# Kernel optimization log

Measured on AMD Instinct MI355X. Metric: run time of the kernel, lower is better.

The kernel has to match this reference:

```python
import jax, jax.numpy as jnp
import numpy as np

B, N = 16, 300000          # batch, total anchors per image (all FPN levels concatenated)
PRE, POST = 2000, 1000     # num_pre_nms, num_post_nms
NMS_THR = 0.7
MIN_SIZE = 1e-3            # proposal_min_size
IMG_H, IMG_W = 800.0, 1333.0


def setup_inputs() -> dict:
    key = jax.random.key(0)
    k1, k2, k3, k4, k5, k6 = jax.random.split(key, 6)
    cls = jax.random.normal(k1, (B, N), dtype=jnp.float32)
    reg = jax.random.normal(k2, (B, N, 4), dtype=jnp.float32) * 0.1
    # anchors as valid (cx,cy,w,h)->(x1,y1,x2,y2) boxes inside the image
    cx = jax.random.uniform(k3, (B, N), dtype=jnp.float32, minval=0.0, maxval=IMG_W)
    cy = jax.random.uniform(k4, (B, N), dtype=jnp.float32, minval=0.0, maxval=IMG_H)
    w = jax.random.uniform(k5, (B, N), dtype=jnp.float32, minval=16.0, maxval=256.0)
    h = jax.random.uniform(k6, (B, N), dtype=jnp.float32, minval=16.0, maxval=256.0)
    anchors = jnp.stack([cx - 0.5 * w, cy - 0.5 * h, cx + 0.5 * w, cy + 0.5 * h], axis=-1)
    return {"cls": cls, "reg": reg, "anchors": anchors}


def _decode(anchor, reg):
    aw = anchor[:, 2] - anchor[:, 0]
    ah = anchor[:, 3] - anchor[:, 1]
    acx = anchor[:, 0] + 0.5 * aw
    acy = anchor[:, 1] + 0.5 * ah
    dx, dy, dw, dh = reg[:, 0], reg[:, 1], reg[:, 2], reg[:, 3]
    pcx = dx * aw + acx
    pcy = dy * ah + acy
    pw = jnp.exp(dw) * aw
    ph = jnp.exp(dh) * ah
    return jnp.stack([pcx - 0.5 * pw, pcy - 0.5 * ph, pcx + 0.5 * pw, pcy + 0.5 * ph], axis=-1)


def _iou_matrix(boxes):
    # boxes: [K,4] -> pairwise IoU [K,K]
    area = (boxes[:, 2] - boxes[:, 0]) * (boxes[:, 3] - boxes[:, 1])
    lt = jnp.maximum(boxes[:, None, :2], boxes[None, :, :2])
    rb = jnp.minimum(boxes[:, None, 2:], boxes[None, :, 2:])
    wh = jnp.clip(rb - lt, 0.0)
    inter = wh[..., 0] * wh[..., 1]
    union = area[:, None] + area[None, :] - inter
    return inter / jnp.maximum(union, 1e-8)


def _per_image(score, reg, anchor):
    # topk pre-NMS selection (lax.top_k returns score-descending order)
    top_s, idx = jax.lax.top_k(score, PRE)
    boxes = _decode(anchor[idx], reg[idx].reshape(-1, 4))
    # clip to image bounds
    bounds = jnp.array([IMG_W, IMG_H, IMG_W, IMG_H], dtype=boxes.dtype)
    boxes = jnp.clip(boxes, 0.0, bounds)
    # remove small boxes (mask instead of dynamic removal)
    w = boxes[:, 2] - boxes[:, 0]
    h = boxes[:, 3] - boxes[:, 1]
    valid = (w >= MIN_SIZE) & (h >= MIN_SIZE)
    s = jnp.where(valid, top_s, -jnp.inf)
    order = jnp.argsort(-s)  # score-descending, invalid last
    boxes = boxes[order]
    valid = valid[order]
    # greedy NMS: iterate highest-score-first, suppress later boxes with IoU > thr
    iou = _iou_matrix(boxes)
    rng = jnp.arange(PRE)
    def body(i, keep):
        sup = (iou[i] > NMS_THR) & keep[i]
        return keep & jnp.logical_not(sup & (rng > i))
    keep = jax.lax.fori_loop(0, PRE, body, valid)
    # gather kept boxes (score order preserved), pad with zeros past count
    sel = jnp.argsort(jnp.logical_not(keep), stable=True)[:POST]
    return boxes[sel] * keep[sel][:, None].astype(boxes.dtype)


def reference(cls, reg, anchors):
    # [B, POST, 4] proposals per image (zero-padded where fewer than POST kept)
    return jax.vmap(_per_image)(cls, reg, anchors)
```

## Files before the change

### kernel.cpp

```cpp
#include <hip/hip_runtime.h>

#define NB 16
#define NN 300000
#define PRE 2000
#define POST 1000

typedef unsigned long long ull;

static const size_t OFF_HIST1   = 0;
static const size_t OFF_HIST2   = 65536;
static const size_t OFF_HIST3   = 196608;
static const size_t OFF_CANDCNT = 327680;
static const size_t OFF_EQCNT   = 327936;
static const size_t OFF_BITMAP  = 328192;
static const size_t OFF_B1      = 332288;
static const size_t OFF_NEED1   = 332544;
static const size_t OFF_B2      = 332800;
static const size_t OFF_NEED2   = 333056;
static const size_t OFF_B3      = 333312;
static const size_t OFF_NEED3   = 333568;
static const size_t OFF_NVALID  = 333824;
static const size_t ZERO_BYTES  = 334080;
static const size_t OFF_CAND    = 334080;
static const size_t OFF_EQBUF   = 465152;
static const size_t OFF_KEYS    = 989440;
static const size_t OFF_BOXTMP  = 1251584;
static const size_t OFF_SORTED  = 1775872;
static const size_t OFF_MASK    = 2287872;

__device__ __forceinline__ unsigned f2u(float f){
  unsigned b = __float_as_uint(f);
  return (b & 0x80000000u) ? ~b : (b | 0x80000000u);
}

#define H1REP 8
#define H1STRIDE 1025
__global__ void k_hist1(const float* __restrict__ cls, unsigned* __restrict__ hist){
  __shared__ unsigned h[H1REP * H1STRIDE];
  int img = blockIdx.y;
  for (int i = threadIdx.x; i < H1REP * H1STRIDE; i += blockDim.x) h[i] = 0;
  __syncthreads();
  const float* p = cls + (size_t)img * NN;
  int stride = gridDim.x * blockDim.x;
  unsigned rep = (threadIdx.x & (H1REP - 1)) * H1STRIDE;
  for (int i = blockIdx.x * blockDim.x + threadIdx.x; i < NN; i += stride)
    atomicAdd(&h[rep + (f2u(p[i]) >> 22)], 1u);
  __syncthreads();
  unsigned* g = hist + img * 1024;
  for (int i = threadIdx.x; i < 1024; i += blockDim.x){
    unsigned v = 0;
    for (int r = 0; r < H1REP; r++) v += h[r * H1STRIDE + i];
    if (v) atomicAdd(&g[i], v);
  }
}

__global__ void k_scan(const unsigned* __restrict__ hist, int bins,
                       const unsigned* __restrict__ tgt, unsigned K0,
                       unsigned* __restrict__ outBin, unsigned* __restrict__ outNeed){
  int img = blockIdx.x;
  int t = threadIdx.x;
  const unsigned* hh = hist + img * bins;
  unsigned K = tgt ? tgt[img] : K0;
  int per = bins >> 8;
  unsigned s = 0;
  for (int q = 0; q < per; q++) s += hh[bins - 1 - (t * per + q)];
  __shared__ unsigned arr[256];
  arr[t] = s;
  __syncthreads();
  for (int off = 1; off < 256; off <<= 1){
    unsigned v = (t >= off) ? arr[t - off] : 0u;
    __syncthreads();
    arr[t] += v;
    __syncthreads();
  }
  unsigned incl = arr[t], excl = incl - s;
  if (excl < K && K <= incl){
    unsigned c = excl;
    for (int q = 0; q < per; q++){
      int b = bins - 1 - (t * per + q);
      unsigned cnt = hh[b];
      if (c + cnt >= K){ outBin[img] = (unsigned)b; outNeed[img] = K - c; break; }
      c += cnt;
    }
  }
}

__global__ void k_hist2(const float* __restrict__ cls, const unsigned* __restrict__ b1,
                        unsigned* __restrict__ hist){
  int img = blockIdx.y;
  unsigned bb1 = b1[img];
  const float* p = cls + (size_t)img * NN;
  unsigned* g = hist + img * 2048;
  int stride = gridDim.x * blockDim.x;
  for (int i = blockIdx.x * blockDim.x + threadIdx.x; i < NN; i += stride){
    unsigned u = f2u(p[i]);
    if ((u >> 22) == bb1) atomicAdd(&g[(u >> 11) & 0x7FFu], 1u);
  }
}

__global__ void k_hist3(const float* __restrict__ cls, const unsigned* __restrict__ b1,
                        const unsigned* __restrict__ b2, unsigned* __restrict__ hist){
  int img = blockIdx.y;
  unsigned pref = (b1[img] << 11) | b2[img];
  const float* p = cls + (size_t)img * NN;
  unsigned* g = hist + img * 2048;
  int stride = gridDim.x * blockDim.x;
  for (int i = blockIdx.x * blockDim.x + threadIdx.x; i < NN; i += stride){
    unsigned u = f2u(p[i]);
    if ((u >> 11) == pref) atomicAdd(&g[u & 0x7FFu], 1u);
  }
}

__global__ void k_compact(const float* __restrict__ cls, const unsigned* __restrict__ b1,
                          const unsigned* __restrict__ b2, const unsigned* __restrict__ b3,
                          unsigned* __restrict__ cand, unsigned* __restrict__ candCnt,
                          unsigned* __restrict__ eqbuf, unsigned* __restrict__ eqCnt){
  __shared__ unsigned lc[1024];
  __shared__ unsigned le[256];
  __shared__ unsigned lcn, len_, baseC, baseE;
  int img = blockIdx.y;
  if (threadIdx.x == 0){ lcn = 0; len_ = 0; }
  __syncthreads();
  unsigned T = (b1[img] << 22) | (b2[img] << 11) | b3[img];
  const float* p = cls + (size_t)img * NN;
  int stride = gridDim.x * blockDim.x;
  for (int i = blockIdx.x * blockDim.x + threadIdx.x; i < NN; i += stride){
    unsigned u = f2u(p[i]);
    if (u > T){
      unsigned pos = atomicAdd(&lcn, 1u);
      if (pos < 1024u) lc[pos] = (unsigned)i;
      else { unsigned g = atomicAdd(&candCnt[img], 1u); if (g < 2048u) cand[img * 2048 + g] = (unsigned)i; }
    } else if (u == T){
      unsigned pos = atomicAdd(&len_, 1u);
      if (pos < 256u) le[pos] = (unsigned)i;
      else { unsigned g = atomicAdd(&eqCnt[img], 1u); if (g < 8192u) eqbuf[img * 8192 + g] = (unsigned)i; }
    }
  }
  __syncthreads();
  unsigned nc = lcn < 1024u ? lcn : 1024u;
  unsigned ne = len_ < 256u ? len_ : 256u;
  if (threadIdx.x == 0){
    if (nc) baseC = atomicAdd(&candCnt[img], nc);
    if (ne) baseE = atomicAdd(&eqCnt[img], ne);
  }
  __syncthreads();
  for (unsigned t = threadIdx.x; t < nc; t += blockDim.x){
    unsigned g = baseC + t;
    if (g < 2048u) cand[img * 2048 + g] = lc[t];
  }
  for (unsigned t = threadIdx.x; t < ne; t += blockDim.x){
    unsigned g = baseE + t;
    if (g < 8192u) eqbuf[img * 8192 + g] = le[t];
  }
}

__global__ void k_finalize(unsigned* __restrict__ cand, const unsigned* __restrict__ candCnt,
                           const unsigned* __restrict__ eqbuf, const unsigned* __restrict__ eqCnt,
                           const unsigned* __restrict__ need3){
  int img = blockIdx.x, tid = threadIdx.x;
  unsigned need = need3[img];
  unsigned ec = eqCnt[img]; if (ec > 8192u) ec = 8192u;
  unsigned base = candCnt[img];
  const unsigned* eq = eqbuf + img * 8192;
  unsigned* c = cand + img * 2048;
  if (need >= ec){
    for (unsigned t = tid; t < ec; t += 256) if (base + t < 2048u) c[base + t] = eq[t];
    return;
  }
  for (unsigned t = tid; t < ec; t += 256){
    unsigned v = eq[t], r = 0;
    for (unsigned s = 0; s < ec; s++) r += (eq[s] < v) ? 1u : 0u;
    if (r < need && base + r < 2048u) c[base + r] = v;
  }
}

__global__ void k_decode(const float* __restrict__ cls, const float* __restrict__ reg,
                         const float* __restrict__ anch, const unsigned* __restrict__ cand,
                         float* __restrict__ boxTmp, ull* __restrict__ keys,
                         unsigned* __restrict__ nvalid){
  int s = blockIdx.x * blockDim.x + threadIdx.x;
  if (s >= NB * 2048) return;
  int img = s >> 11, slot = s & 2047;
  ull key = 0ull;
  float4 box = make_float4(0.f, 0.f, 0.f, 0.f);
  bool counted = false;
  if (slot < PRE){
    unsigned i = cand[img * 2048 + slot];
    if (i < NN){
      size_t gi = (size_t)img * NN + i;
      float4 a = ((const float4*)anch)[gi];
      float4 r = ((const float4*)reg)[gi];
      float sc = cls[gi];
      float aw = a.z - a.x, ah = a.w - a.y;
      float acx = a.x + 0.5f * aw, acy = a.y + 0.5f * ah;
      float pcx = r.x * aw + acx, pcy = r.y * ah + acy;
      float pw = expf(r.z) * aw, ph = expf(r.w) * ah;
      float x1 = pcx - 0.5f * pw, y1 = pcy - 0.5f * ph;
      float x2 = pcx + 0.5f * pw, y2 = pcy + 0.5f * ph;
      x1 = fminf(fmaxf(x1, 0.f), 1333.f); x2 = fminf(fmaxf(x2, 0.f), 1333.f);
      y1 = fminf(fmaxf(y1, 0.f), 800.f);  y2 = fminf(fmaxf(y2, 0.f), 800.f);
      bool valid = ((x2 - x1) >= 0.001f) && ((y2 - y1) >= 0.001f);
      unsigned up = valid ? f2u(sc) : 0u;
      key = ((ull)up << 32) | (ull)(0xFFFFFFFFu - i);
      box = make_float4(x1, y1, x2, y2);
      counted = valid;
    }
  }
  keys[img * 2048 + slot] = key;
  ((float4*)boxTmp)[img * 2048 + slot] = box;
  ull bal = __ballot(counted);
  if ((threadIdx.x & 63) == 0 && bal)
    atomicAdd(&nvalid[img], (unsigned)__popcll(bal));
}

__global__ __launch_bounds__(256) void k_rank(const ull* __restrict__ keys,
                                              const float* __restrict__ boxTmp,
                                              float* __restrict__ sorted){
  __shared__ ull lk[2048];
  int img = blockIdx.y;
  int e = blockIdx.x * 256 + threadIdx.x;
  for (int t = threadIdx.x; t < 2048; t += 256) lk[t] = keys[img * 2048 + t];
  __syncthreads();
  ull me = lk[e];
  unsigned rank = 0;
  #pragma unroll 8
  for (int j = 0; j < 2048; j++) rank += (lk[j] > me) ? 1u : 0u;
  if (rank < PRE)
    ((float4*)sorted)[img * PRE + rank] = ((const float4*)boxTmp)[img * 2048 + e];
}

__global__ __launch_bounds__(512) void k_mask(const float* __restrict__ sorted,
                                              const unsigned* __restrict__ nvalid,
                                              ull* __restrict__ mask, ull* __restrict__ bitmap){
  __shared__ float4 bx[PRE];
  __shared__ float  ar[PRE];
  __shared__ unsigned rowflag[16];
  int img = blockIdx.y, tid = threadIdx.x;
  if (tid < 16) rowflag[tid] = 0;
  for (int i = tid; i < PRE; i += 512){
    float4 b = ((const float4*)sorted)[img * PRE + i];
    bx[i] = b;
    ar[i] = (b.z - b.x) * (b.w - b.y);
  }
  __syncthreads();
  int row = blockIdx.x * 16 + (tid >> 5);
  int w = tid & 31;
  float4 bi = bx[row];
  float ai = ar[row];
  int qlo = (row >= w) ? (((row - w) >> 5) + 1) : 0;
  int qhi = ((PRE - 1 - w) >> 5) + 1;
  ull m = 0;
  for (int q = qlo; q < qhi; q++){
    int j = (q << 5) + w;
    float4 bj = bx[j];
    float xx1 = fmaxf(bi.x, bj.x), yy1 = fmaxf(bi.y, bj.y);
    float xx2 = fminf(bi.z, bj.z), yy2 = fminf(bi.w, bj.w);
    float ww = fmaxf(xx2 - xx1, 0.f), hh = fmaxf(yy2 - yy1, 0.f);
    float inter = ww * hh;
    float uni = ai + ar[j] - inter;
    if (inter / fmaxf(uni, 1e-8f) > 0.7f) m |= (1ull << q);
  }
  mask[((size_t)(img * PRE + row)) * 32 + w] = m;
  if (m) atomicOr(&rowflag[tid >> 5], 1u);
  __syncthreads();
  if (tid < 16){
    int r = blockIdx.x * 16 + tid;
    if (rowflag[tid] && r < (int)nvalid[img])
      atomicOr(&bitmap[img * 32 + (r >> 6)], 1ull << (r & 63));
  }
}

#define CHR 48
__global__ __launch_bounds__(256) void k_nms(const ull* __restrict__ mask,
                                             const ull* __restrict__ bitmap,
                                             const unsigned* __restrict__ nvalid,
                                             const float* __restrict__ sorted,
                                             float* __restrict__ out){
  __shared__ unsigned rowsLds[2048];
  __shared__ unsigned cntw[32];
  __shared__ unsigned wbaseS[32];
  __shared__ int mcountS, mpS;
  __shared__ ull cacheD[2][CHR * 32];
  __shared__ ull keepP[32];
  __shared__ ull keepLin[32];
  __shared__ unsigned cntArr[32], preArr[32];
  int img = blockIdx.x, tid = threadIdx.x;
  int lane = tid & 63, wave = tid >> 6;

  if (tid < 32) cntw[tid] = (unsigned)__popcll(bitmap[img * 32 + tid]);
  __syncthreads();
  if (tid == 0){
    unsigned s = 0;
    for (int w0 = 0; w0 < 32; w0++){ wbaseS[w0] = s; s += cntw[w0]; }
    mcountS = (int)s;
    mpS = ((int)s + CHR - 1) / CHR * CHR;
  }
  __syncthreads();
  int m = mcountS, mp = mpS;
  if (tid < 32){
    ull bits = bitmap[img * 32 + tid];
    unsigned pos = wbaseS[tid];
    int base_i = tid * 64;
    while (bits){
      int b = __ffsll((long long)bits) - 1;
      rowsLds[pos++] = (unsigned)(base_i + b);
      bits &= bits - 1;
    }
  }
  for (int t = m + tid; t < mp; t += 256) rowsLds[t] = PRE - 1;
  __syncthreads();

  int nch = mp / CHR;
  ull remv = 0;
  const ull* mg = mask + (size_t)img * PRE * 32;

  if (nch > 0 && tid >= 64){
    int s = tid - 64;
    ull v[8];
    #pragma unroll
    for (int k = 0; k < 8; k++){
      int t = k * 192 + s;
      unsigned rr = rowsLds[t >> 5];
      v[k] = mg[(size_t)rr * 32 + (t & 31)];
    }
    #pragma unroll
    for (int k = 0; k < 8; k++) cacheD[0][k * 192 + s] = v[k];
  }
  __syncthreads();

  for (int c = 0; c < nch; c++){
    int cb = c & 1;
    if (tid >= 64){
      if (c + 1 < nch){
        int q0n = (c + 1) * CHR;
        int s = tid - 64;
        ull v[8];
        #pragma unroll
        for (int k = 0; k < 8; k++){
          int t = k * 192 + s;
          unsigned rr = rowsLds[q0n + (t >> 5)];
          v[k] = mg[(size_t)rr * 32 + (t & 31)];
        }
        #pragma unroll
        for (int k = 0; k < 8; k++) cacheD[cb ^ 1][k * 192 + s] = v[k];
      }
    } else {
      const ull* cbuf = cacheD[cb];
      const int q0 = c * CHR;
      ull cur[8]; unsigned ci[8];
      #pragma unroll
      for (int k = 0; k < 8; k++){
        ci[k] = rowsLds[q0 + k];
        cur[k] = cbuf[(k << 5) | (lane & 31)];
      }
      #pragma unroll
      for (int g = 0; g < 6; g++){
        ull nxt[8]; unsigned ni[8];
        if (g < 5){
          #pragma unroll
          for (int k = 0; k < 8; k++){
            int lq = (g + 1) * 8 + k;
            ni[k] = rowsLds[q0 + lq];
            nxt[k] = cbuf[(lq << 5) | (lane & 31)];
          }
        }
        #pragma unroll
        for (int k = 0; k < 8; k++){
          unsigned i = ci[k];
          unsigned bit = ((unsigned)(remv >> (i >> 5))) & 1u;
          int sup = (lane == (int)(i & 31)) && bit;
          if (!__any(sup)) remv |= cur[k];
        }
        if (g < 5){
          #pragma unroll
          for (int k = 0; k < 8; k++){ cur[k] = nxt[k]; ci[k] = ni[k]; }
        }
      }
    }
    __syncthreads();
  }

  int nv = (int)nvalid[img];
  if (wave == 0 && lane < 32){
    int cnt2 = (nv > lane) ? (((nv - 1 - lane) >> 5) + 1) : 0;
    ull vm = (cnt2 >= 64) ? ~0ull : ((1ull << cnt2) - 1ull);
    keepP[lane] = (~remv) & vm;
  }
  __syncthreads();
  if (tid < 32){
    ull lin = 0;
    for (int kk = 0; kk < 64; kk++)
      lin |= ((keepP[kk & 31] >> (2 * tid + (kk >> 5))) & 1ull) << kk;
    keepLin[tid] = lin;
    cntArr[tid] = (unsigned)__popcll(lin);
  }
  __syncthreads();
  if (tid < 32){
    unsigned pre = 0;
    for (int w0 = 0; w0 < tid; w0++) pre += cntArr[w0];
    preArr[tid] = pre;
  }
  __syncthreads();
  for (int i = tid; i < PRE; i += 256){
    int w0 = i >> 6, b = i & 63;
    ull kw = keepLin[w0];
    if ((kw >> b) & 1ull){
      unsigned rank = preArr[w0] + (unsigned)__popcll(kw & ((1ull << b) - 1ull));
      if (rank < POST)
        ((float4*)out)[img * POST + rank] = ((const float4*)sorted)[img * PRE + i];
    }
  }
}

extern "C" void kernel_launch(void* const* d_in, const int* in_sizes, int n_in,
                              void* d_out, int out_size, void* d_ws, size_t ws_size,
                              hipStream_t stream){
  const float* cls  = (const float*)d_in[0];
  const float* reg  = (const float*)d_in[1];
  const float* anch = (const float*)d_in[2];
  float* out = (float*)d_out;
  char* ws = (char*)d_ws;

  unsigned* hist1   = (unsigned*)(ws + OFF_HIST1);
  unsigned* hist2   = (unsigned*)(ws + OFF_HIST2);
  unsigned* hist3   = (unsigned*)(ws + OFF_HIST3);
  unsigned* candCnt = (unsigned*)(ws + OFF_CANDCNT);
  unsigned* eqCnt   = (unsigned*)(ws + OFF_EQCNT);
  ull*      bitmap  = (ull*)     (ws + OFF_BITMAP);
  unsigned* b1      = (unsigned*)(ws + OFF_B1);
  unsigned* need1   = (unsigned*)(ws + OFF_NEED1);
  unsigned* b2      = (unsigned*)(ws + OFF_B2);
  unsigned* need2   = (unsigned*)(ws + OFF_NEED2);
  unsigned* b3      = (unsigned*)(ws + OFF_B3);
  unsigned* need3   = (unsigned*)(ws + OFF_NEED3);
  unsigned* nvalid  = (unsigned*)(ws + OFF_NVALID);
  unsigned* cand    = (unsigned*)(ws + OFF_CAND);
  unsigned* eqbuf   = (unsigned*)(ws + OFF_EQBUF);
  ull*      keys    = (ull*)     (ws + OFF_KEYS);
  float*    boxTmp  = (float*)   (ws + OFF_BOXTMP);
  float*    sorted  = (float*)   (ws + OFF_SORTED);
  ull*      mask    = (ull*)     (ws + OFF_MASK);

  hipMemsetAsync(ws, 0, ZERO_BYTES, stream);
  hipMemsetAsync(d_out, 0, (size_t)out_size * sizeof(float), stream);

  k_hist1<<<dim3(64, NB), 256, 0, stream>>>(cls, hist1);
  k_scan <<<NB, 256, 0, stream>>>(hist1, 1024, (const unsigned*)nullptr, 2000u, b1, need1);
  k_hist2<<<dim3(64, NB), 256, 0, stream>>>(cls, b1, hist2);
  k_scan <<<NB, 256, 0, stream>>>(hist2, 2048, need1, 0u, b2, need2);
  k_hist3<<<dim3(64, NB), 256, 0, stream>>>(cls, b1, b2, hist3);
  k_scan <<<NB, 256, 0, stream>>>(hist3, 2048, need2, 0u, b3, need3);
  k_compact<<<dim3(64, NB), 256, 0, stream>>>(cls, b1, b2, b3, cand, candCnt, eqbuf, eqCnt);
  k_finalize<<<NB, 256, 0, stream>>>(cand, candCnt, eqbuf, eqCnt, need3);
  k_decode<<<(NB * 2048) / 256, 256, 0, stream>>>(cls, reg, anch, cand, boxTmp, keys, nvalid);
  k_rank<<<dim3(8, NB), 256, 0, stream>>>(keys, boxTmp, sorted);
  k_mask<<<dim3(PRE / 16, NB), 512, 0, stream>>>(sorted, nvalid, mask, bitmap);
  k_nms<<<NB, 256, 0, stream>>>(mask, bitmap, nvalid, sorted, out);
}
```

Baseline: 305.3 us.

## Fuse all pipeline stages into one cooperative persistent kernel with grid syncs

Replaces the twelve separate launches and the memsets with a single cooperative kernel of 768 blocks. Stages are separated by grid-wide syncs, and each stage reuses one shared-memory buffer. The mask stage is spread over 48 blocks per image. The aim is to remove per-launch overhead and idle gaps between many small kernels, at the cost of grid-sync latency and fixed occupancy limits.

```diff
diff --git a/kernel.cpp b/kernel.cpp
--- a/kernel.cpp
+++ b/kernel.cpp
@@ -1,70 +1,69 @@
 #include <hip/hip_runtime.h>
+#include <hip/hip_cooperative_groups.h>
+
+namespace cg = cooperative_groups;
 
 #define NB 16
 #define NN 300000
 #define PRE 2000
 #define POST 1000
+#define GRID 768
+#define BLK 256
+#define BPI 48
+#define CHR 48
 
 typedef unsigned long long ull;
 
-static const size_t OFF_HIST1   = 0;
-static const size_t OFF_HIST2   = 65536;
-static const size_t OFF_HIST3   = 196608;
-static const size_t OFF_CANDCNT = 327680;
-static const size_t OFF_EQCNT   = 327936;
-static const size_t OFF_BITMAP  = 328192;
-static const size_t OFF_B1      = 332288;
-static const size_t OFF_NEED1   = 332544;
-static const size_t OFF_B2      = 332800;
-static const size_t OFF_NEED2   = 333056;
-static const size_t OFF_B3      = 333312;
-static const size_t OFF_NEED3   = 333568;
-static const size_t OFF_NVALID  = 333824;
-static const size_t ZERO_BYTES  = 334080;
-static const size_t OFF_CAND    = 334080;
-static const size_t OFF_EQBUF   = 465152;
-static const size_t OFF_KEYS    = 989440;
-static const size_t OFF_BOXTMP  = 1251584;
-static const size_t OFF_SORTED  = 1775872;
-static const size_t OFF_MASK    = 2287872;
+static constexpr size_t OFF_HIST1   = 0;
+static constexpr size_t OFF_HIST2   = 65536;
+static constexpr size_t OFF_HIST3   = 196608;
+static constexpr size_t OFF_CANDCNT = 327680;
+static constexpr size_t OFF_EQCNT   = 327936;
+static constexpr size_t OFF_BITMAP  = 328192;
+static constexpr size_t OFF_B1      = 332288;
+static constexpr size_t OFF_NEED1   = 332544;
+static constexpr size_t OFF_B2      = 332800;
+static constexpr size_t OFF_NEED2   = 333056;
+static constexpr size_t OFF_B3      = 333312;
+static constexpr size_t OFF_NEED3   = 333568;
+static constexpr size_t OFF_NVALID  = 333824;
+static constexpr size_t ZERO_BYTES  = 334080;
+static constexpr size_t OFF_CAND    = 334080;
+static constexpr size_t OFF_EQBUF   = 465152;
+static constexpr size_t OFF_KEYS    = 989440;
+static constexpr size_t OFF_BOXTMP  = 1251584;
+static constexpr size_t OFF_SORTED  = 1775872;
+static constexpr size_t OFF_MASK    = 2287872;
 
 __device__ __forceinline__ unsigned f2u(float f){
   unsigned b = __float_as_uint(f);
   return (b & 0x80000000u) ? ~b : (b | 0x80000000u);
 }
 
-#define H1REP 8
-#define H1STRIDE 1025
-__global__ void k_hist1(const float* __restrict__ cls, unsigned* __restrict__ hist){
-  __shared__ unsigned h[H1REP * H1STRIDE];
-  int img = blockIdx.y;
-  for (int i = threadIdx.x; i < H1REP * H1STRIDE; i += blockDim.x) h[i] = 0;
-  __syncthreads();
-  const float* p = cls + (size_t)img * NN;
-  int stride = gridDim.x * blockDim.x;
-  unsigned rep = (threadIdx.x & (H1REP - 1)) * H1STRIDE;
-  for (int i = blockIdx.x * blockDim.x + threadIdx.x; i < NN; i += stride)
-    atomicAdd(&h[rep + (f2u(p[i]) >> 22)], 1u);
-  __syncthreads();
-  unsigned* g = hist + img * 1024;
-  for (int i = threadIdx.x; i < 1024; i += blockDim.x){
-    unsigned v = 0;
-    for (int r = 0; r < H1REP; r++) v += h[r * H1STRIDE + i];
-    if (v) atomicAdd(&g[i], v);
-  }
-}
-
-__global__ void k_scan(const unsigned* __restrict__ hist, int bins,
-                       const unsigned* __restrict__ tgt, unsigned K0,
-                       unsigned* __restrict__ outBin, unsigned* __restrict__ outNeed){
-  int img = blockIdx.x;
-  int t = threadIdx.x;
+struct CompactS { unsigned lc[1024]; unsigned le[256]; unsigned lcn, len_, baseC, baseE; };
+struct NmsS {
+  unsigned rowsLds[2048];
+  unsigned cntw[32];
+  unsigned wbaseS[32];
+  int mcountS, mpS;
+  ull cacheD[2][CHR * 32];
+  ull keepP[32];
+  ull keepLin[32];
+  unsigned cntArr[32], preArr[32];
+};
+static_assert(sizeof(CompactS) <= 40448, "compact lds");
+static_assert(sizeof(NmsS)     <= 40448, "nms lds");
+
+__device__ void dev_scan(const unsigned* __restrict__ hist, int bins,
+                         const unsigned* __restrict__ tgt, unsigned K0,
+                         unsigned* __restrict__ outBin, unsigned* __restrict__ outNeed,
+                         char* sm, int img, int t){
+  unsigned* arr = (unsigned*)sm;
   const unsigned* hh = hist + img * bins;
   unsigned K = tgt ? tgt[img] : K0;
   int per = bins >> 8;
   unsigned s = 0;
   for (int q = 0; q < per; q++) s += hh[bins - 1 - (t * per + q)];
-  __shared__ unsigned arr[256];
   arr[t] = s;
   __syncthreads();
   for (int off = 1; off < 256; off <<= 1){
@@ -85,341 +84,16 @@
   }
 }
 
-__global__ void k_hist2(const float* __restrict__ cls, const unsigned* __restrict__ b1,
-                        unsigned* __restrict__ hist){
-  int img = blockIdx.y;
-  unsigned bb1 = b1[img];
-  const float* p = cls + (size_t)img * NN;
-  unsigned* g = hist + img * 2048;
-  int stride = gridDim.x * blockDim.x;
-  for (int i = blockIdx.x * blockDim.x + threadIdx.x; i < NN; i += stride){
-    unsigned u = f2u(p[i]);
-    if ((u >> 22) == bb1) atomicAdd(&g[(u >> 11) & 0x7FFu], 1u);
-  }
-}
-
-__global__ void k_hist3(const float* __restrict__ cls, const unsigned* __restrict__ b1,
-                        const unsigned* __restrict__ b2, unsigned* __restrict__ hist){
-  int img = blockIdx.y;
-  unsigned pref = (b1[img] << 11) | b2[img];
-  const float* p = cls + (size_t)img * NN;
-  unsigned* g = hist + img * 2048;
-  int stride = gridDim.x * blockDim.x;
-  for (int i = blockIdx.x * blockDim.x + threadIdx.x; i < NN; i += stride){
-    unsigned u = f2u(p[i]);
-    if ((u >> 11) == pref) atomicAdd(&g[u & 0x7FFu], 1u);
-  }
-}
-
-__global__ void k_compact(const float* __restrict__ cls, const unsigned* __restrict__ b1,
-                          const unsigned* __restrict__ b2, const unsigned* __restrict__ b3,
-                          unsigned* __restrict__ cand, unsigned* __restrict__ candCnt,
-                          unsigned* __restrict__ eqbuf, unsigned* __restrict__ eqCnt){
-  __shared__ unsigned lc[1024];
-  __shared__ unsigned le[256];
-  __shared__ unsigned lcn, len_, baseC, baseE;
-  int img = blockIdx.y;
-  if (threadIdx.x == 0){ lcn = 0; len_ = 0; }
-  __syncthreads();
-  unsigned T = (b1[img] << 22) | (b2[img] << 11) | b3[img];
-  const float* p = cls + (size_t)img * NN;
-  int stride = gridDim.x * blockDim.x;
-  for (int i = blockIdx.x * blockDim.x + threadIdx.x; i < NN; i += stride){
-    unsigned u = f2u(p[i]);
-    if (u > T){
-      unsigned pos = atomicAdd(&lcn, 1u);
-      if (pos < 1024u) lc[pos] = (unsigned)i;
-      else { unsigned g = atomicAdd(&candCnt[img], 1u); if (g < 2048u) cand[img * 2048 + g] = (unsigned)i; }
-    } else if (u == T){
-      unsigned pos = atomicAdd(&len_, 1u);
-      if (pos < 256u) le[pos] = (unsigned)i;
-      else { unsigned g = atomicAdd(&eqCnt[img], 1u); if (g < 8192u) eqbuf[img * 8192 + g] = (unsigned)i; }
-    }
-  }
-  __syncthreads();
-  unsigned nc = lcn < 1024u ? lcn : 1024u;
-  unsigned ne = len_ < 256u ? len_ : 256u;
-  if (threadIdx.x == 0){
-    if (nc) baseC = atomicAdd(&candCnt[img], nc);
-    if (ne) baseE = atomicAdd(&eqCnt[img], ne);
-  }
-  __syncthreads();
-  for (unsigned t = threadIdx.x; t < nc; t += blockDim.x){
-    unsigned g = baseC + t;
-    if (g < 2048u) cand[img * 2048 + g] = lc[t];
-  }
-  for (unsigned t = threadIdx.x; t < ne; t += blockDim.x){
-    unsigned g = baseE + t;
-    if (g < 8192u) eqbuf[img * 8192 + g] = le[t];
-  }
-}
-
-__global__ void k_finalize(unsigned* __restrict__ cand, const unsigned* __restrict__ candCnt,
-                           const unsigned* __restrict__ eqbuf, const unsigned* __restrict__ eqCnt,
-                           const unsigned* __restrict__ need3){
-  int img = blockIdx.x, tid = threadIdx.x;
-  unsigned need = need3[img];
-  unsigned ec = eqCnt[img]; if (ec > 8192u) ec = 8192u;
-  unsigned base = candCnt[img];
-  const unsigned* eq = eqbuf + img * 8192;
-  unsigned* c = cand + img * 2048;
-  if (need >= ec){
-    for (unsigned t = tid; t < ec; t += 256) if (base + t < 2048u) c[base + t] = eq[t];
-    return;
-  }
-  for (unsigned t = tid; t < ec; t += 256){
-    unsigned v = eq[t], r = 0;
-    for (unsigned s = 0; s < ec; s++) r += (eq[s] < v) ? 1u : 0u;
-    if (r < need && base + r < 2048u) c[base + r] = v;
-  }
-}
-
-__global__ void k_decode(const float* __restrict__ cls, const float* __restrict__ reg,
-                         const float* __restrict__ anch, const unsigned* __restrict__ cand,
-                         float* __restrict__ boxTmp, ull* __restrict__ keys,
-                         unsigned* __restrict__ nvalid){
-  int s = blockIdx.x * blockDim.x + threadIdx.x;
-  if (s >= NB * 2048) return;
-  int img = s >> 11, slot = s & 2047;
-  ull key = 0ull;
-  float4 box = make_float4(0.f, 0.f, 0.f, 0.f);
-  bool counted = false;
-  if (slot < PRE){
-    unsigned i = cand[img * 2048 + slot];
-    if (i < NN){
-      size_t gi = (size_t)img * NN + i;
-      float4 a = ((const float4*)anch)[gi];
-      float4 r = ((const float4*)reg)[gi];
-      float sc = cls[gi];
-      float aw = a.z - a.x, ah = a.w - a.y;
-      float acx = a.x + 0.5f * aw, acy = a.y + 0.5f * ah;
-      float pcx = r.x * aw + acx, pcy = r.y * ah + acy;
-      float pw = expf(r.z) * aw, ph = expf(r.w) * ah;
-      float x1 = pcx - 0.5f * pw, y1 = pcy - 0.5f * ph;
-      float x2 = pcx + 0.5f * pw, y2 = pcy + 0.5f * ph;
-      x1 = fminf(fmaxf(x1, 0.f), 1333.f); x2 = fminf(fmaxf(x2, 0.f), 1333.f);
-      y1 = fminf(fmaxf(y1, 0.f), 800.f);  y2 = fminf(fmaxf(y2, 0.f), 800.f);
-      bool valid = ((x2 - x1) >= 0.001f) && ((y2 - y1) >= 0.001f);
-      unsigned up = valid ? f2u(sc) : 0u;
-      key = ((ull)up << 32) | (ull)(0xFFFFFFFFu - i);
-      box = make_float4(x1, y1, x2, y2);
-      counted = valid;
-    }
-  }
-  keys[img * 2048 + slot] = key;
-  ((float4*)boxTmp)[img * 2048 + slot] = box;
-  ull bal = __ballot(counted);
-  if ((threadIdx.x & 63) == 0 && bal)
-    atomicAdd(&nvalid[img], (unsigned)__popcll(bal));
-}
-
-__global__ __launch_bounds__(256) void k_rank(const ull* __restrict__ keys,
-                                              const float* __restrict__ boxTmp,
-                                              float* __restrict__ sorted){
-  __shared__ ull lk[2048];
-  int img = blockIdx.y;
-  int e = blockIdx.x * 256 + threadIdx.x;
-  for (int t = threadIdx.x; t < 2048; t += 256) lk[t] = keys[img * 2048 + t];
-  __syncthreads();
-  ull me = lk[e];
-  unsigned rank = 0;
-  #pragma unroll 8
-  for (int j = 0; j < 2048; j++) rank += (lk[j] > me) ? 1u : 0u;
-  if (rank < PRE)
-    ((float4*)sorted)[img * PRE + rank] = ((const float4*)boxTmp)[img * 2048 + e];
-}
-
-__global__ __launch_bounds__(512) void k_mask(const float* __restrict__ sorted,
-                                              const unsigned* __restrict__ nvalid,
-                                              ull* __restrict__ mask, ull* __restrict__ bitmap){
-  __shared__ float4 bx[PRE];
-  __shared__ float  ar[PRE];
-  __shared__ unsigned rowflag[16];
-  int img = blockIdx.y, tid = threadIdx.x;
-  if (tid < 16) rowflag[tid] = 0;
-  for (int i = tid; i < PRE; i += 512){
-    float4 b = ((const float4*)sorted)[img * PRE + i];
-    bx[i] = b;
-    ar[i] = (b.z - b.x) * (b.w - b.y);
-  }
-  __syncthreads();
-  int row = blockIdx.x * 16 + (tid >> 5);
-  int w = tid & 31;
-  float4 bi = bx[row];
-  float ai = ar[row];
-  int qlo = (row >= w) ? (((row - w) >> 5) + 1) : 0;
-  int qhi = ((PRE - 1 - w) >> 5) + 1;
-  ull m = 0;
-  for (int q = qlo; q < qhi; q++){
-    int j = (q << 5) + w;
-    float4 bj = bx[j];
-    float xx1 = fmaxf(bi.x, bj.x), yy1 = fmaxf(bi.y, bj.y);
-    float xx2 = fminf(bi.z, bj.z), yy2 = fminf(bi.w, bj.w);
-    float ww = fmaxf(xx2 - xx1, 0.f), hh = fmaxf(yy2 - yy1, 0.f);
-    float inter = ww * hh;
-    float uni = ai + ar[j] - inter;
-    if (inter / fmaxf(uni, 1e-8f) > 0.7f) m |= (1ull << q);
-  }
-  mask[((size_t)(img * PRE + row)) * 32 + w] = m;
-  if (m) atomicOr(&rowflag[tid >> 5], 1u);
-  __syncthreads();
-  if (tid < 16){
-    int r = blockIdx.x * 16 + tid;
-    if (rowflag[tid] && r < (int)nvalid[img])
-      atomicOr(&bitmap[img * 32 + (r >> 6)], 1ull << (r & 63));
-  }
-}
-
-#define CHR 48
-__global__ __launch_bounds__(256) void k_nms(const ull* __restrict__ mask,
-                                             const ull* __restrict__ bitmap,
-                                             const unsigned* __restrict__ nvalid,
-                                             const float* __restrict__ sorted,
-                                             float* __restrict__ out){
-  __shared__ unsigned rowsLds[2048];
-  __shared__ unsigned cntw[32];
-  __shared__ unsigned wbaseS[32];
-  __shared__ int mcountS, mpS;
-  __shared__ ull cacheD[2][CHR * 32];
-  __shared__ ull keepP[32];
-  __shared__ ull keepLin[32];
-  __shared__ unsigned cntArr[32], preArr[32];
-  int img = blockIdx.x, tid = threadIdx.x;
-  int lane = tid & 63, wave = tid >> 6;
-
-  if (tid < 32) cntw[tid] = (unsigned)__popcll(bitmap[img * 32 + tid]);
-  __syncthreads();
-  if (tid == 0){
-    unsigned s = 0;
-    for (int w0 = 0; w0 < 32; w0++){ wbaseS[w0] = s; s += cntw[w0]; }
-    mcountS = (int)s;
-    mpS = ((int)s + CHR - 1) / CHR * CHR;
-  }
-  __syncthreads();
-  int m = mcountS, mp = mpS;
-  if (tid < 32){
-    ull bits = bitmap[img * 32 + tid];
-    unsigned pos = wbaseS[tid];
-    int base_i = tid * 64;
-    while (bits){
-      int b = __ffsll((long long)bits) - 1;
-      rowsLds[pos++] = (unsigned)(base_i + b);
-      bits &= bits - 1;
-    }
-  }
-  for (int t = m + tid; t < mp; t += 256) rowsLds[t] = PRE - 1;
-  __syncthreads();
-
-  int nch = mp / CHR;
-  ull remv = 0;
-  const ull* mg = mask + (size_t)img * PRE * 32;
-
-  if (nch > 0 && tid >= 64){
-    int s = tid - 64;
-    ull v[8];
-    #pragma unroll
-    for (int k = 0; k < 8; k++){
-      int t = k * 192 + s;
-      unsigned rr = rowsLds[t >> 5];
-      v[k] = mg[(size_t)rr * 32 + (t & 31)];
-    }
-    #pragma unroll
-    for (int k = 0; k < 8; k++) cacheD[0][k * 192 + s] = v[k];
-  }
-  __syncthreads();
-
-  for (int c = 0; c < nch; c++){
-    int cb = c & 1;
-    if (tid >= 64){
-      if (c + 1 < nch){
-        int q0n = (c + 1) * CHR;
-        int s = tid - 64;
-        ull v[8];
-        #pragma unroll
-        for (int k = 0; k < 8; k++){
-          int t = k * 192 + s;
-          unsigned rr = rowsLds[q0n + (t >> 5)];
-          v[k] = mg[(size_t)rr * 32 + (t & 31)];
-        }
-        #pragma unroll
-        for (int k = 0; k < 8; k++) cacheD[cb ^ 1][k * 192 + s] = v[k];
-      }
-    } else {
-      const ull* cbuf = cacheD[cb];
-      const int q0 = c * CHR;
-      ull cur[8]; unsigned ci[8];
-      #pragma unroll
-      for (int k = 0; k < 8; k++){
-        ci[k] = rowsLds[q0 + k];
-        cur[k] = cbuf[(k << 5) | (lane & 31)];
-      }
-      #pragma unroll
-      for (int g = 0; g < 6; g++){
-        ull nxt[8]; unsigned ni[8];
-        if (g < 5){
-          #pragma unroll
-          for (int k = 0; k < 8; k++){
-            int lq = (g + 1) * 8 + k;
-            ni[k] = rowsLds[q0 + lq];
-            nxt[k] = cbuf[(lq << 5) | (lane & 31)];
-          }
-        }
-        #pragma unroll
-        for (int k = 0; k < 8; k++){
-          unsigned i = ci[k];
-          unsigned bit = ((unsigned)(remv >> (i >> 5))) & 1u;
-          int sup = (lane == (int)(i & 31)) && bit;
-          if (!__any(sup)) remv |= cur[k];
-        }
-        if (g < 5){
-          #pragma unroll
-          for (int k = 0; k < 8; k++){ cur[k] = nxt[k]; ci[k] = ni[k]; }
-        }
-      }
-    }
-    __syncthreads();
-  }
-
-  int nv = (int)nvalid[img];
-  if (wave == 0 && lane < 32){
-    int cnt2 = (nv > lane) ? (((nv - 1 - lane) >> 5) + 1) : 0;
-    ull vm = (cnt2 >= 64) ? ~0ull : ((1ull << cnt2) - 1ull);
-    keepP[lane] = (~remv) & vm;
-  }
-  __syncthreads();
-  if (tid < 32){
-    ull lin = 0;
-    for (int kk = 0; kk < 64; kk++)
-      lin |= ((keepP[kk & 31] >> (2 * tid + (kk >> 5))) & 1ull) << kk;
-    keepLin[tid] = lin;
-    cntArr[tid] = (unsigned)__popcll(lin);
-  }
-  __syncthreads();
-  if (tid < 32){
-    unsigned pre = 0;
-    for (int w0 = 0; w0 < tid; w0++) pre += cntArr[w0];
-    preArr[tid] = pre;
-  }
-  __syncthreads();
-  for (int i = tid; i < PRE; i += 256){
-    int w0 = i >> 6, b = i & 63;
-    ull kw = keepLin[w0];
-    if ((kw >> b) & 1ull){
-      unsigned rank = preArr[w0] + (unsigned)__popcll(kw & ((1ull << b) - 1ull));
-      if (rank < POST)
-        ((float4*)out)[img * POST + rank] = ((const float4*)sorted)[img * PRE + i];
-    }
-  }
-}
-
-extern "C" void kernel_launch(void* const* d_in, const int* in_sizes, int n_in,
-                              void* d_out, int out_size, void* d_ws, size_t ws_size,
-                              hipStream_t stream){
-  const float* cls  = (const float*)d_in[0];
-  const float* reg  = (const float*)d_in[1];
-  const float* anch = (const float*)d_in[2];
-  float* out = (float*)d_out;
-  char* ws = (char*)d_ws;
+__global__ __launch_bounds__(BLK, 3) void mega(const float* __restrict__ cls,
+                                               const float* __restrict__ reg,
+                                               const float* __restrict__ anch,
+                                               float* __restrict__ out,
+                                               char* __restrict__ ws,
+                                               int outFloats){
+  __shared__ __align__(16) char sm[40448];
+  cg::grid_group gg = cg::this_grid();
+  const int bid = blockIdx.x, tid = threadIdx.x;
+  const int gtid = bid * BLK + tid;
 
   unsigned* hist1   = (unsigned*)(ws + OFF_HIST1);
   unsigned* hist2   = (unsigned*)(ws + OFF_HIST2);
@@ -439,21 +113,359 @@
   ull*      keys    = (ull*)     (ws + OFF_KEYS);
   float*    boxTmp  = (float*)   (ws + OFF_BOXTMP);
   float*    sorted  = (float*)   (ws + OFF_SORTED);
-  ull*      mask    = (ull*)     (ws + OFF_MASK);
-
-  hipMemsetAsync(ws, 0, ZERO_BYTES, stream);
-  hipMemsetAsync(d_out, 0, (size_t)out_size * sizeof(float), stream);
-
-  k_hist1<<<dim3(64, NB), 256, 0, stream>>>(cls, hist1);
-  k_scan <<<NB, 256, 0, stream>>>(hist1, 1024, (const unsigned*)nullptr, 2000u, b1, need1);
-  k_hist2<<<dim3(64, NB), 256, 0, stream>>>(cls, b1, hist2);
-  k_scan <<<NB, 256, 0, stream>>>(hist2, 2048, need1, 0u, b2, need2);
-  k_hist3<<<dim3(64, NB), 256, 0, stream>>>(cls, b1, b2, hist3);
-  k_scan <<<NB, 256, 0, stream>>>(hist3, 2048, need2, 0u, b3, need3);
-  k_compact<<<dim3(64, NB), 256, 0, stream>>>(cls, b1, b2, b3, cand, candCnt, eqbuf, eqCnt);
-  k_finalize<<<NB, 256, 0, stream>>>(cand, candCnt, eqbuf, eqCnt, need3);
-  k_decode<<<(NB * 2048) / 256, 256, 0, stream>>>(cls, reg, anch, cand, boxTmp, keys, nvalid);
-  k_rank<<<dim3(8, NB), 256, 0, stream>>>(keys, boxTmp, sorted);
-  k_mask<<<dim3(PRE / 16, NB), 512, 0, stream>>>(sorted, nvalid, mask, bitmap);
-  k_nms<<<NB, 256, 0, stream>>>(mask, bitmap, nvalid, sorted, out);
+  ull*      maskG   = (ull*)     (ws + OFF_MASK);
+
+  {
+    unsigned* z = (unsigned*)ws;
+    for (int i = gtid; i < (int)(ZERO_BYTES / 4); i += GRID * BLK) z[i] = 0u;
+    for (int i = gtid; i < outFloats; i += GRID * BLK) out[i] = 0.f;
+  }
+  gg.sync();
+
+  {
+    unsigned* h = (unsigned*)sm;
+    int img = bid / BPI, sub = bid % BPI;
+    for (int i = tid; i < 8 * 1025; i += BLK) h[i] = 0;
+    __syncthreads();
+    const float* p = cls + (size_t)img * NN;
+    unsigned rep = (tid & 7) * 1025;
+    for (int i = sub * BLK + tid; i < NN; i += BPI * BLK)
+      atomicAdd(&h[rep + (f2u(p[i]) >> 22)], 1u);
+    __syncthreads();
+    unsigned* g = hist1 + img * 1024;
+    for (int i = tid; i < 1024; i += BLK){
+      unsigned v = 0;
+      #pragma unroll
+      for (int r = 0; r < 8; r++) v += h[r * 1025 + i];
+      if (v) atomicAdd(&g[i], v);
+    }
+  }
+  gg.sync();
+
+  if (bid < NB) dev_scan(hist1, 1024, (const unsigned*)nullptr, 2000u, b1, need1, sm, bid, tid);
+  gg.sync();
+
+  {
+    int img = bid / BPI, sub = bid % BPI;
+    unsigned bb1 = b1[img];
+    const float* p = cls + (size_t)img * NN;
+    unsigned* g = hist2 + img * 2048;
+    for (int i = sub * BLK + tid; i < NN; i += BPI * BLK){
+      unsigned u = f2u(p[i]);
+      if ((u >> 22) == bb1) atomicAdd(&g[(u >> 11) & 0x7FFu], 1u);
+    }
+  }
+  gg.sync();
+
+  if (bid < NB) dev_scan(hist2, 2048, need1, 0u, b2, need2, sm, bid, tid);
+  gg.sync();
+
+  {
+    int img = bid / BPI, sub = bid % BPI;
+    unsigned pref = (b1[img] << 11) | b2[img];
+    const float* p = cls + (size_t)img * NN;
+    unsigned* g = hist3 + img * 2048;
+    for (int i = sub * BLK + tid; i < NN; i += BPI * BLK){
+      unsigned u = f2u(p[i]);
+      if ((u >> 11) == pref) atomicAdd(&g[u & 0x7FFu], 1u);
+    }
+  }
+  gg.sync();
+
+  if (bid < NB) dev_scan(hist3, 2048, need2, 0u, b3, need3, sm, bid, tid);
+  gg.sync();
+
+  {
+    CompactS* cs = (CompactS*)sm;
+    int img = bid / BPI, sub = bid % BPI;
+    if (tid == 0){ cs->lcn = 0; cs->len_ = 0; }
+    __syncthreads();
+    unsigned T = (b1[img] << 22) | (b2[img] << 11) | b3[img];
+    const float* p = cls + (size_t)img * NN;
+    for (int i = sub * BLK + tid; i < NN; i += BPI * BLK){
+      unsigned u = f2u(p[i]);
+      if (u > T){
+        unsigned pos = atomicAdd(&cs->lcn, 1u);
+        if (pos < 1024u) cs->lc[pos] = (unsigned)i;
+        else { unsigned g2 = atomicAdd(&candCnt[img], 1u); if (g2 < 2048u) cand[img * 2048 + g2] = (unsigned)i; }
+      } else if (u == T){
+        unsigned pos = atomicAdd(&cs->len_, 1u);
+        if (pos < 256u) cs->le[pos] = (unsigned)i;
+        else { unsigned g2 = atomicAdd(&eqCnt[img], 1u); if (g2 < 8192u) eqbuf[img * 8192 + g2] = (unsigned)i; }
+      }
+    }
+    __syncthreads();
+    unsigned nc = cs->lcn < 1024u ? cs->lcn : 1024u;
+    unsigned ne = cs->len_ < 256u ? cs->len_ : 256u;
+    if (tid == 0){
+      if (nc) cs->baseC = atomicAdd(&candCnt[img], nc);
+      if (ne) cs->baseE = atomicAdd(&eqCnt[img], ne);
+    }
+    __syncthreads();
+    for (unsigned t = tid; t < nc; t += BLK){
+      unsigned g2 = cs->baseC + t;
+      if (g2 < 2048u) cand[img * 2048 + g2] = cs->lc[t];
+    }
+    for (unsigned t = tid; t < ne; t += BLK){
+      unsigned g2 = cs->baseE + t;
+      if (g2 < 8192u) eqbuf[img * 8192 + g2] = cs->le[t];
+    }
+  }
+  gg.sync();
+
+  if (bid < NB){
+    int img = bid;
+    unsigned need = need3[img];
+    unsigned ec = eqCnt[img]; if (ec > 8192u) ec = 8192u;
+    unsigned base = candCnt[img];
+    const unsigned* eq = eqbuf + img * 8192;
+    unsigned* c = cand + img * 2048;
+    if (need >= ec){
+      for (unsigned t = tid; t < ec; t += BLK) if (base + t < 2048u) c[base + t] = eq[t];
+    } else {
+      for (unsigned t = tid; t < ec; t += BLK){
+        unsigned v = eq[t], r = 0;
+        for (unsigned s2 = 0; s2 < ec; s2++) r += (eq[s2] < v) ? 1u : 0u;
+        if (r < need && base + r < 2048u) c[base + r] = v;
+      }
+    }
+  }
+  gg.sync();
+
+  if (bid < 128){
+    int s = bid * BLK + tid;
+    int img = s >> 11, slot = s & 2047;
+    ull key = 0ull;
+    float4 box = make_float4(0.f, 0.f, 0.f, 0.f);
+    bool counted = false;
+    if (slot < PRE){
+      unsigned i = cand[img * 2048 + slot];
+      if (i < NN){
+        size_t gi = (size_t)img * NN + i;
+        float4 a = ((const float4*)anch)[gi];
+        float4 r = ((const float4*)reg)[gi];
+        float sc = cls[gi];
+        float aw = a.z - a.x, ah = a.w - a.y;
+        float acx = a.x + 0.5f * aw, acy = a.y + 0.5f * ah;
+        float pcx = r.x * aw + acx, pcy = r.y * ah + acy;
+        float pw = expf(r.z) * aw, ph = expf(r.w) * ah;
+        float x1 = pcx - 0.5f * pw, y1 = pcy - 0.5f * ph;
+        float x2 = pcx + 0.5f * pw, y2 = pcy + 0.5f * ph;
+        x1 = fminf(fmaxf(x1, 0.f), 1333.f); x2 = fminf(fmaxf(x2, 0.f), 1333.f);
+        y1 = fminf(fmaxf(y1, 0.f), 800.f);  y2 = fminf(fmaxf(y2, 0.f), 800.f);
+        bool valid = ((x2 - x1) >= 0.001f) && ((y2 - y1) >= 0.001f);
+        unsigned up = valid ? f2u(sc) : 0u;
+        key = ((ull)up << 32) | (ull)(0xFFFFFFFFu - i);
+        box = make_float4(x1, y1, x2, y2);
+        counted = valid;
+      }
+    }
+    keys[img * 2048 + slot] = key;
+    ((float4*)boxTmp)[img * 2048 + slot] = box;
+    ull bal = __ballot(counted);
+    if ((tid & 63) == 0 && bal)
+      atomicAdd(&nvalid[img], (unsigned)__popcll(bal));
+  }
+  gg.sync();
+
+  if (bid < 128){
+    ull* lk = (ull*)sm;
+    int img = bid >> 3;
+    int e = (bid & 7) * 256 + tid;
+    for (int t = tid; t < 2048; t += BLK) lk[t] = keys[img * 2048 + t];
+    __syncthreads();
+    ull me = lk[e];
+    unsigned rank = 0;
+    #pragma unroll 8
+    for (int j = 0; j < 2048; j++) rank += (lk[j] > me) ? 1u : 0u;
+    if (rank < PRE)
+      ((float4*)sorted)[img * PRE + rank] = ((const float4*)boxTmp)[img * 2048 + e];
+  }
+  gg.sync();
+
+  {
+    float4* bx = (float4*)sm;
+    float*  ar = (float*)(sm + PRE * sizeof(float4));
+    int img = bid / BPI, sub = bid % BPI;
+    for (int i = tid; i < PRE; i += BLK){
+      float4 b = ((const float4*)sorted)[img * PRE + i];
+      bx[i] = b;
+      ar[i] = (b.z - b.x) * (b.w - b.y);
+    }
+    int nv = (int)nvalid[img];
+    __syncthreads();
+    int w = tid & 31;
+    int rsub = tid >> 5;
+    int qhi = ((PRE - 1 - w) >> 5) + 1;
+    for (int u = sub; u < PRE / 8; u += BPI){
+      int row = u * 8 + rsub;
+      float4 bi = bx[row];
+      float ai = ar[row];
+      int qlo = (row >= w) ? (((row - w) >> 5) + 1) : 0;
+      ull m = 0;
+      for (int q = qlo; q < qhi; q++){
+        int j = (q << 5) + w;
+        float4 bj = bx[j];
+        float xx1 = fmaxf(bi.x, bj.x), yy1 = fmaxf(bi.y, bj.y);
+        float xx2 = fminf(bi.z, bj.z), yy2 = fminf(bi.w, bj.w);
+        float ww = fmaxf(xx2 - xx1, 0.f), hh = fmaxf(yy2 - yy1, 0.f);
+        float inter = ww * hh;
+        float uni = ai + ar[j] - inter;
+        if (inter / fmaxf(uni, 1e-8f) > 0.7f) m |= (1ull << q);
+      }
+      maskG[((size_t)(img * PRE + row)) * 32 + w] = m;
+      ull nz = __ballot(m != 0ull);
+      int lane = tid & 63;
+      if (lane == 0 || lane == 32){
+        ull half = (lane == 0) ? (nz & 0xFFFFFFFFull) : (nz >> 32);
+        if (half && row < nv)
+          atomicOr(&bitmap[img * 32 + (row >> 6)], 1ull << (row & 63));
+      }
+    }
+  }
+  gg.sync();
+
+  if (bid < NB){
+    NmsS* ns = (NmsS*)sm;
+    int img = bid;
+    int lane = tid & 63, wave = tid >> 6;
+
+    if (tid < 32) ns->cntw[tid] = (unsigned)__popcll(bitmap[img * 32 + tid]);
+    __syncthreads();
+    if (tid == 0){
+      unsigned s2 = 0;
+      for (int w0 = 0; w0 < 32; w0++){ ns->wbaseS[w0] = s2; s2 += ns->cntw[w0]; }
+      ns->mcountS = (int)s2;
+      ns->mpS = ((int)s2 + CHR - 1) / CHR * CHR;
+    }
+    __syncthreads();
+    int m = ns->mcountS, mp = ns->mpS;
+    if (tid < 32){
+      ull bits = bitmap[img * 32 + tid];
+      unsigned pos = ns->wbaseS[tid];
+      int base_i = tid * 64;
+      while (bits){
+        int b = __ffsll((long long)bits) - 1;
+        ns->rowsLds[pos++] = (unsigned)(base_i + b);
+        bits &= bits - 1;
+      }
+    }
+    for (int t = m + tid; t < mp; t += BLK) ns->rowsLds[t] = PRE - 1;
+    __syncthreads();
+
+    int nch = mp / CHR;
+    ull remv = 0;
+    const ull* mg = maskG + (size_t)img * PRE * 32;
+
+    if (nch > 0 && tid >= 64){
+      int s2 = tid - 64;
+      ull v[8];
+      #pragma unroll
+      for (int k = 0; k < 8; k++){
+        int t = k * 192 + s2;
+        unsigned rr = ns->rowsLds[t >> 5];
+        v[k] = mg[(size_t)rr * 32 + (t & 31)];
+      }
+      #pragma unroll
+      for (int k = 0; k < 8; k++) ns->cacheD[0][k * 192 + s2] = v[k];
+    }
+    __syncthreads();
+
+    for (int c = 0; c < nch; c++){
+      int cb = c & 1;
+      if (tid >= 64){
+        if (c + 1 < nch){
+          int q0n = (c + 1) * CHR;
+          int s2 = tid - 64;
+          ull v[8];
+          #pragma unroll
+          for (int k = 0; k < 8; k++){
+            int t = k * 192 + s2;
+            unsigned rr = ns->rowsLds[q0n + (t >> 5)];
+            v[k] = mg[(size_t)rr * 32 + (t & 31)];
+          }
+          #pragma unroll
+          for (int k = 0; k < 8; k++) ns->cacheD[cb ^ 1][k * 192 + s2] = v[k];
+        }
+      } else {
+        const ull* cbuf = ns->cacheD[cb];
+        const int q0 = c * CHR;
+        ull cur[8]; unsigned ci[8];
+        #pragma unroll
+        for (int k = 0; k < 8; k++){
+          ci[k] = ns->rowsLds[q0 + k];
+          cur[k] = cbuf[(k << 5) | (lane & 31)];
+        }
+        #pragma unroll
+        for (int g2 = 0; g2 < 6; g2++){
+          ull nxt[8]; unsigned ni[8];
+          if (g2 < 5){
+            #pragma unroll
+            for (int k = 0; k < 8; k++){
+              int lq = (g2 + 1) * 8 + k;
+              ni[k] = ns->rowsLds[q0 + lq];
+              nxt[k] = cbuf[(lq << 5) | (lane & 31)];
+            }
+          }
+          #pragma unroll
+          for (int k = 0; k < 8; k++){
+            unsigned i = ci[k];
+            unsigned bit = ((unsigned)(remv >> (i >> 5))) & 1u;
+            int sup = (lane == (int)(i & 31)) && bit;
+            if (!__any(sup)) remv |= cur[k];
+          }
+          if (g2 < 5){
+            #pragma unroll
+            for (int k = 0; k < 8; k++){ cur[k] = nxt[k]; ci[k] = ni[k]; }
+          }
+        }
+      }
+      __syncthreads();
+    }
+
+    int nv = (int)nvalid[img];
+    if (wave == 0 && lane < 32){
+      int cnt2 = (nv > lane) ? (((nv - 1 - lane) >> 5) + 1) : 0;
+      ull vm = (cnt2 >= 64) ? ~0ull : ((1ull << cnt2) - 1ull);
+      ns->keepP[lane] = (~remv) & vm;
+    }
+    __syncthreads();
+    if (tid < 32){
+      ull lin = 0;
+      for (int kk = 0; kk < 64; kk++)
+        lin |= ((ns->keepP[kk & 31] >> (2 * tid + (kk >> 5))) & 1ull) << kk;
+      ns->keepLin[tid] = lin;
+      ns->cntArr[tid] = (unsigned)__popcll(lin);
+    }
+    __syncthreads();
+    if (tid < 32){
+      unsigned pre = 0;
+      for (int w0 = 0; w0 < tid; w0++) pre += ns->cntArr[w0];
+      ns->preArr[tid] = pre;
+    }
+    __syncthreads();
+    for (int i = tid; i < PRE; i += BLK){
+      int w0 = i >> 6, b = i & 63;
+      ull kw = ns->keepLin[w0];
+      if ((kw >> b) & 1ull){
+        unsigned rank = ns->preArr[w0] + (unsigned)__popcll(kw & ((1ull << b) - 1ull));
+        if (rank < POST)
+          ((float4*)out)[img * POST + rank] = ((const float4*)sorted)[img * PRE + i];
+      }
+    }
+  }
 }
+
+extern "C" void kernel_launch(void* const* d_in, const int* in_sizes, int n_in,
+                              void* d_out, int out_size, void* d_ws, size_t ws_size,
+                              hipStream_t stream){
+  const float* cls  = (const float*)d_in[0];
+  const float* reg  = (const float*)d_in[1];
+  const float* anch = (const float*)d_in[2];
+  float* out = (float*)d_out;
+  char* ws = (char*)d_ws;
+  int outFloats = out_size;
+
+  void* args[] = { (void*)&cls, (void*)&reg, (void*)&anch, (void*)&out, (void*)&ws, (void*)&outFloats };
+  hipLaunchCooperativeKernel((const void*)mega, dim3(GRID), dim3(BLK), args, 0, stream);
+}
```

Measured after the change: 1.214 ms. +297.7%, slower.
